# Optimization experiments

Measured on AMD Instinct MI355X. Metric: run time of the kernel, lower is better.

The kernel has to match this reference:

```python
import jax, jax.numpy as jnp
import numpy as np

N_NODES = 50000


def gcn_conv(x, W, b, src, dst, n_nodes):
    """PyG GCNConv: h = x @ W; symmetric-normalized aggregation with self-loops; + bias."""
    h = x @ W  # [N, F_out]
    ones = jnp.ones(src.shape[0], dtype=h.dtype)
    # degree including the self-loop (edge weight 1)
    deg = jax.ops.segment_sum(ones, dst, num_segments=n_nodes) + 1.0
    dinv = jax.lax.rsqrt(deg)  # deg >= 1, always valid
    norm = dinv[src] * dinv[dst]  # [E]
    msgs = h[src] * norm[:, None]  # [E, F_out]
    agg = jax.ops.segment_sum(msgs, dst, num_segments=n_nodes)
    agg = agg + h * (dinv * dinv)[:, None]  # self-loop contribution, norm = dinv_i^2
    return agg + b


def setup_inputs() -> dict:
    key = jax.random.key(0)
    ks = jax.random.split(key, 8)
    n, f_in, f_hid, f_out, n_edges = N_NODES, 128, 128, 40, 800000
    x = jax.random.normal(ks[0], (n, f_in), dtype=jnp.float32)
    edge_index = jax.random.randint(ks[1], (2, n_edges), 0, n, dtype=jnp.int64)
    new_edge_indexs = jax.random.randint(ks[2], (2, 1000), 0, n, dtype=jnp.int64)
    # Glorot init like PyG defaults
    s1 = (6.0 / (f_in + f_hid)) ** 0.5
    s2 = (6.0 / (f_hid + f_out)) ** 0.5
    W1 = jax.random.uniform(ks[3], (f_in, f_hid), jnp.float32, -s1, s1)
    b1 = jnp.zeros((f_hid,), jnp.float32)
    W2 = jax.random.uniform(ks[4], (f_hid, f_out), jnp.float32, -s2, s2)
    b2 = jnp.zeros((f_out,), jnp.float32)
    return {"x": x, "W1": W1, "b1": b1, "W2": W2, "b2": b2,
            "edge_index": edge_index, "new_edge_indexs": new_edge_indexs}


def reference(x, W1, b1, W2, b2, edge_index, new_edge_indexs):
    src, dst = edge_index[0], edge_index[1]
    h = gcn_conv(x, W1, b1, src, dst, N_NODES)
    h = jax.nn.relu(h)
    # dropout(p=0.5) is identity in eval mode (training=False)
    h = gcn_conv(h, W2, b2, src, dst, N_NODES)
    return jax.nn.log_softmax(h, axis=-1)
```

## Files before the change

### kernel.cpp

```cpp
#include <hip/hip_runtime.h>
#include <hip/hip_bf16.h>

#define N_NODES 50000
#define N_EDGES 800000
#define F_IN    128
#define F_HID   128
#define F_OUT   40
#define N_TILES (N_NODES / 16)

#define NBIN      98
#define BIN_SHIFT 9
#define EPB       1024
#define CAP       32
#define GBIN_CAP  9216

#define CVT_BLOCKS ((F_IN * F_HID + 48 * F_HID) / 256)

typedef __attribute__((ext_vector_type(8))) short bf16x8;
typedef __attribute__((ext_vector_type(4))) float f32x4;

__device__ __forceinline__ float2 unpack_bf2(unsigned u) {
    float2 r;
    r.x = __uint_as_float(u << 16);
    r.y = __uint_as_float(u & 0xffff0000u);
    return r;
}
__device__ __forceinline__ unsigned pack_bf2(float x, float y) {
    union { unsigned u; __hip_bfloat16 h[2]; } cv;
    cv.h[0] = __float2bfloat16(x);
    cv.h[1] = __float2bfloat16(y);
    return cv.u;
}
__device__ __forceinline__ short bfraw(float v) {
    __hip_bfloat16 h = __float2bfloat16(v);
    return *(short*)&h;
}
__device__ __forceinline__ float bf16u_to_f32(unsigned short us) {
    return __uint_as_float(((unsigned)us) << 16);
}
__device__ __forceinline__ unsigned f32_to_h16(float v) {
    _Float16 h = (_Float16)v;
    return (unsigned)*(unsigned short*)&h;
}
__device__ __forceinline__ float h16_to_f32(unsigned bits) {
    unsigned short us = (unsigned short)bits;
    _Float16 h = *(_Float16*)&us;
    return (float)h;
}

__device__ __forceinline__ int ld_src(const unsigned int* w, int is64, int e) {
    return is64 ? (int)w[2 * e] : (int)w[e];
}
__device__ __forceinline__ int ld_dst(const unsigned int* w, int is64, int e) {
    return is64 ? (int)w[2 * (N_EDGES + e)] : (int)w[N_EDGES + e];
}

__global__ void k_init(const unsigned int* __restrict__ ew,
                       const float* __restrict__ W1, const float* __restrict__ W2,
                       __hip_bfloat16* __restrict__ w1t, __hip_bfloat16* __restrict__ w2t,
                       int* __restrict__ flag, int* __restrict__ gcnt) {
    int b = blockIdx.x, t = threadIdx.x;
    if (b < CVT_BLOCKS) {
        int idx = b * 256 + t;
        if (idx < F_IN * F_HID) {
            int n = idx >> 7, k = idx & 127;
            w1t[idx] = __float2bfloat16(W1[k * F_HID + n]);
        } else {
            int j = idx - F_IN * F_HID;
            int n = j >> 7, k = j & 127;
            w2t[j] = __float2bfloat16(n < F_OUT ? W2[k * F_OUT + n] : 0.f);
        }
        return;
    }
    __shared__ int nz;
    if (t == 0) nz = 0;
    __syncthreads();
    int local = 0;
    for (int i = t; i < 4096; i += 256)
        if (ew[2 * i + 1] != 0u) local = 1;
    if (local) atomicOr(&nz, 1);
    if (t < NBIN) gcnt[t] = 0;
    __syncthreads();
    if (t == 0) flag[0] = (nz == 0) ? 1 : 0;
}

__global__ void k_bin(const unsigned int* __restrict__ ew, const int* __restrict__ flag,
                      int* __restrict__ gcnt, unsigned* __restrict__ gbin) {
    __shared__ unsigned buf[NBIN][CAP];
    __shared__ int cnt[NBIN];
    __shared__ int base[NBIN];
    int t = threadIdx.x;
    for (int i = t; i < NBIN; i += 256) cnt[i] = 0;
    __syncthreads();
    int is64 = flag[0];
    int e0 = blockIdx.x * EPB;
    int n = min(EPB, N_EDGES - e0);
    for (int i = t; i < n; i += 256) {
        int e = e0 + i;
        int s = ld_src(ew, is64, e), d = ld_dst(ew, is64, e);
        unsigned rec = (unsigned)s | ((unsigned)d << 16);
        int b = d >> BIN_SHIFT;
        int c = atomicAdd(&cnt[b], 1);
        if (c < CAP) buf[b][c] = rec;
        else {
            int g = atomicAdd(&gcnt[b], 1);
            gbin[(size_t)b * GBIN_CAP + g] = rec;
        }
    }
    __syncthreads();
    if (t < NBIN) {
        int m = min(cnt[t], CAP);
        base[t] = atomicAdd(&gcnt[t], m);
        cnt[t] = m;
    }
    __syncthreads();
    int wave = t >> 6, lane = t & 63;
    for (int b = wave; b < NBIN; b += 4) {
        int m = cnt[b], bs = base[b];
        for (int i = lane; i < m; i += 64)
            gbin[(size_t)b * GBIN_CAP + bs + i] = buf[b][i];
    }
}

__global__ void k_passB1(const int* __restrict__ gcnt, const unsigned* __restrict__ gbin,
                         int* __restrict__ rowptr, float* __restrict__ dinv) {
    __shared__ int c[512];
    __shared__ int s2[256];
    __shared__ int gall[NBIN];
    __shared__ int bbase;
    int t = threadIdx.x;
    int b = blockIdx.x;
    c[t] = 0; c[t + 256] = 0;
    if (t < NBIN) gall[t] = gcnt[t];
    __syncthreads();
    if (t == 0) {
        int s = 0;
        for (int i = 0; i < b; i++) s += gall[i];
        bbase = s;
    }
    int n = gall[b];
    const unsigned* rec = gbin + (size_t)b * GBIN_CAP;
    int base512 = b << BIN_SHIFT;
    for (int i = t; i < n; i += 256)
        atomicAdd(&c[(int)(rec[i] >> 16) - base512], 1);
    __syncthreads();
    int a0 = c[2 * t], a1 = c[2 * t + 1];
    s2[t] = a0 + a1;
    __syncthreads();
    for (int off = 1; off < 256; off <<= 1) {
        int u = (t >= off) ? s2[t - off] : 0;
        __syncthreads();
        s2[t] += u;
        __syncthreads();
    }
    int ebase = bbase + s2[t] - a0 - a1;
    int i0 = base512 + 2 * t, i1 = i0 + 1;
    if (i0 < N_NODES) { rowptr[i0] = ebase;      dinv[i0] = rsqrtf((float)a0 + 1.f); }
    if (i1 < N_NODES) { rowptr[i1] = ebase + a0; dinv[i1] = rsqrtf((float)a1 + 1.f); }
    if (b == 0 && t == 0) rowptr[N_NODES] = N_EDGES;
}

__global__ void k_passB2(const int* __restrict__ gcnt, const unsigned* __restrict__ gbin,
                         const int* __restrict__ rowptr, const float* __restrict__ dinv,
                         unsigned* __restrict__ srcw) {
    __shared__ int pos[512];
    __shared__ float dloc[512];
    int t = threadIdx.x;
    int b = blockIdx.x;
    int base512 = b << BIN_SHIFT;
#pragma unroll
    for (int k = 0; k < 2; k++) {
        int j = t + k * 256;
        int i = base512 + j;
        pos[j]  = (i < N_NODES) ? rowptr[i] : 0;
        dloc[j] = (i < N_NODES) ? dinv[i] : 0.f;
    }
    __syncthreads();
    int n = gcnt[b];
    const unsigned* rec = gbin + (size_t)b * GBIN_CAP;
    for (int i = t; i < n; i += 256) {
        unsigned r = rec[i];
        int s  = (int)(r & 0xFFFFu);
        int dl = (int)(r >> 16) - base512;
        int slot = atomicAdd(&pos[dl], 1);
        float norm = dinv[s] * dloc[dl];
        srcw[slot] = (unsigned)s | (f32_to_h16(norm) << 16);
    }
}

__global__ void k_gemm1m(const float* __restrict__ x,
                         const __hip_bfloat16* __restrict__ w1t,
                         __hip_bfloat16* __restrict__ h1b) {
    int wave = threadIdx.x >> 6, lane = threadIdx.x & 63;
    int tile = blockIdx.x * 4 + wave;
    if (tile >= N_TILES) return;
    int node0 = tile * 16;
    int m = lane & 15, q = lane >> 4;
    bf16x8 A[4];
    const float* arow = x + (size_t)(node0 + m) * F_IN + q * 8;
#pragma unroll
    for (int kt = 0; kt < 4; kt++) {
        float4 f0 = *(const float4*)(arow + kt * 32);
        float4 f1 = *(const float4*)(arow + kt * 32 + 4);
        bf16x8 a;
        a[0] = bfraw(f0.x); a[1] = bfraw(f0.y); a[2] = bfraw(f0.z); a[3] = bfraw(f0.w);
        a[4] = bfraw(f1.x); a[5] = bfraw(f1.y); a[6] = bfraw(f1.z); a[7] = bfraw(f1.w);
        A[kt] = a;
    }
#pragma unroll
    for (int c = 0; c < 8; c++) {
        f32x4 acc = {0.f, 0.f, 0.f, 0.f};
        const __hip_bfloat16* brow = w1t + (size_t)(c * 16 + m) * F_IN + q * 8;
#pragma unroll
        for (int kt = 0; kt < 4; kt++) {
            bf16x8 B = *(const bf16x8*)(brow + kt * 32);
            acc = __builtin_amdgcn_mfma_f32_16x16x32_bf16(A[kt], B, acc, 0, 0, 0);
        }
#pragma unroll
        for (int r = 0; r < 4; r++)
            h1b[(size_t)(node0 + q * 4 + r) * F_HID + c * 16 + m] = __float2bfloat16(acc[r]);
    }
}

__global__ void k_agg1f(const int* __restrict__ rowptr, const unsigned* __restrict__ srcw,
                        const float* __restrict__ dinv, const __hip_bfloat16* __restrict__ h1b,
                        const float* __restrict__ b1, __hip_bfloat16* __restrict__ h1rb) {
    int wave = threadIdx.x >> 6, lane = threadIdx.x & 63;
    int node = blockIdx.x * 4 + wave;
    float di = dinv[node];
    int beg = rowptr[node], end = rowptr[node + 1];
    const unsigned* h1u = (const unsigned*)h1b;
    float2 acc = unpack_bf2(h1u[(size_t)node * 64 + lane]);
    float w0 = di * di;
    acc.x *= w0; acc.y *= w0;
    int e = beg;
    for (; e + 3 < end; e += 4) {
        unsigned p0 = srcw[e], p1 = srcw[e + 1], p2 = srcw[e + 2], p3 = srcw[e + 3];
        unsigned u0 = h1u[(size_t)(p0 & 0xFFFF) * 64 + lane];
        unsigned u1 = h1u[(size_t)(p1 & 0xFFFF) * 64 + lane];
        unsigned u2 = h1u[(size_t)(p2 & 0xFFFF) * 64 + lane];
        unsigned u3 = h1u[(size_t)(p3 & 0xFFFF) * 64 + lane];
        float w0e = h16_to_f32(p0 >> 16);
        float w1e = h16_to_f32(p1 >> 16);
        float w2e = h16_to_f32(p2 >> 16);
        float w3e = h16_to_f32(p3 >> 16);
        float2 v0 = unpack_bf2(u0), v1 = unpack_bf2(u1), v2 = unpack_bf2(u2), v3 = unpack_bf2(u3);
        acc.x += v0.x * w0e + v1.x * w1e + v2.x * w2e + v3.x * w3e;
        acc.y += v0.y * w0e + v1.y * w1e + v2.y * w2e + v3.y * w3e;
    }
    for (; e < end; e++) {
        unsigned p = srcw[e];
        float w = h16_to_f32(p >> 16);
        float2 v = unpack_bf2(h1u[(size_t)(p & 0xFFFF) * 64 + lane]);
        acc.x += v.x * w;
        acc.y += v.y * w;
    }
    float2 bb = ((const float2*)b1)[lane];
    acc.x = fmaxf(acc.x + bb.x, 0.f);
    acc.y = fmaxf(acc.y + bb.y, 0.f);
    ((unsigned*)h1rb)[(size_t)node * 64 + lane] = pack_bf2(acc.x, acc.y);
}

__global__ void k_gemm2m(const __hip_bfloat16* __restrict__ h1rb,
                         const __hip_bfloat16* __restrict__ w2t,
                         __hip_bfloat16* __restrict__ h2b) {
    int wave = threadIdx.x >> 6, lane = threadIdx.x & 63;
    int tile = blockIdx.x * 4 + wave;
    if (tile >= N_TILES) return;
    int node0 = tile * 16;
    int m = lane & 15, q = lane >> 4;
    bf16x8 A[4];
    const __hip_bfloat16* arow = h1rb + (size_t)(node0 + m) * F_HID + q * 8;
#pragma unroll
    for (int kt = 0; kt < 4; kt++)
        A[kt] = *(const bf16x8*)(arow + kt * 32);
#pragma unroll
    for (int c = 0; c < 3; c++) {
        f32x4 acc = {0.f, 0.f, 0.f, 0.f};
        const __hip_bfloat16* brow = w2t + (size_t)(c * 16 + m) * F_HID + q * 8;
#pragma unroll
        for (int kt = 0; kt < 4; kt++) {
            bf16x8 B = *(const bf16x8*)(brow + kt * 32);
            acc = __builtin_amdgcn_mfma_f32_16x16x32_bf16(A[kt], B, acc, 0, 0, 0);
        }
        int col = c * 16 + m;
        if (col < F_OUT) {
#pragma unroll
            for (int r = 0; r < 4; r++)
                h2b[(size_t)(node0 + q * 4 + r) * F_OUT + col] = __float2bfloat16(acc[r]);
        }
    }
}

__global__ void k_agg2f(const int* __restrict__ rowptr, const unsigned* __restrict__ srcw,
                        const float* __restrict__ dinv,
                        const unsigned short* __restrict__ h2b,
                        const float* __restrict__ b2, float* __restrict__ out) {
    int wave = threadIdx.x >> 6, lane = threadIdx.x & 63;
    int node = blockIdx.x * 4 + wave;
    float di = dinv[node];
    int beg = rowptr[node], end = rowptr[node + 1];
    int l = (lane < F_OUT) ? lane : 0;
    float acc = bf16u_to_f32(h2b[(size_t)node * F_OUT + l]) * di * di;
    int e = beg;
    for (; e + 3 < end; e += 4) {
        unsigned p0 = srcw[e], p1 = srcw[e + 1], p2 = srcw[e + 2], p3 = srcw[e + 3];
        float v0 = bf16u_to_f32(h2b[(size_t)(p0 & 0xFFFF) * F_OUT + l]);
        float v1 = bf16u_to_f32(h2b[(size_t)(p1 & 0xFFFF) * F_OUT + l]);
        float v2 = bf16u_to_f32(h2b[(size_t)(p2 & 0xFFFF) * F_OUT + l]);
        float v3 = bf16u_to_f32(h2b[(size_t)(p3 & 0xFFFF) * F_OUT + l]);
        acc += v0 * h16_to_f32(p0 >> 16) + v1 * h16_to_f32(p1 >> 16)
             + v2 * h16_to_f32(p2 >> 16) + v3 * h16_to_f32(p3 >> 16);
    }
    for (; e < end; e++) {
        unsigned p = srcw[e];
        acc += bf16u_to_f32(h2b[(size_t)(p & 0xFFFF) * F_OUT + l]) * h16_to_f32(p >> 16);
    }
    float v = (lane < F_OUT) ? acc + b2[lane] : -INFINITY;
    float m = v;
    for (int off = 32; off; off >>= 1) m = fmaxf(m, __shfl_xor(m, off));
    float ex = (lane < F_OUT) ? __expf(v - m) : 0.f;
    float ssum = ex;
    for (int off = 32; off; off >>= 1) ssum += __shfl_xor(ssum, off);
    float ls = __logf(ssum);
    if (lane < F_OUT)
        out[(size_t)node * F_OUT + lane] = v - m - ls;
}

extern "C" void kernel_launch(void* const* d_in, const int* in_sizes, int n_in,
                              void* d_out, int out_size, void* d_ws, size_t ws_size,
                              hipStream_t stream) {
    const float* x  = (const float*)d_in[0];
    const float* W1 = (const float*)d_in[1];
    const float* b1 = (const float*)d_in[2];
    const float* W2 = (const float*)d_in[3];
    const float* b2 = (const float*)d_in[4];
    const unsigned int* ew = (const unsigned int*)d_in[5];
    float* out = (float*)d_out;

    char* ws = (char*)d_ws;
    int*   flag     = (int*)ws;   ws += 256;
    int*   gcnt     = (int*)ws;   ws += 512;
    float* dinv     = (float*)ws; ws += ((N_NODES * 4 + 255) / 256) * 256;
    int*   rowptr   = (int*)ws;   ws += (((N_NODES + 1) * 4 + 255) / 256) * 256;
    unsigned* gbin  = (unsigned*)ws; ws += (size_t)NBIN * GBIN_CAP * 4;
    unsigned* srcw  = (unsigned*)ws; ws += (size_t)N_EDGES * 4;
    __hip_bfloat16* w1t  = (__hip_bfloat16*)ws; ws += F_IN * F_HID * 2;
    __hip_bfloat16* w2t  = (__hip_bfloat16*)ws; ws += 48 * F_HID * 2;
    __hip_bfloat16* h1b  = (__hip_bfloat16*)ws; ws += (size_t)N_NODES * F_HID * 2;
    __hip_bfloat16* h1rb = (__hip_bfloat16*)ws; ws += (size_t)N_NODES * F_HID * 2;
    __hip_bfloat16* h2b  = (__hip_bfloat16*)ws; ws += (size_t)N_NODES * F_OUT * 2;

    k_init   <<<CVT_BLOCKS + 1, 256, 0, stream>>>(ew, W1, W2, w1t, w2t, flag, gcnt);
    k_bin    <<<(N_EDGES + EPB - 1) / EPB, 256, 0, stream>>>(ew, flag, gcnt, gbin);
    k_passB1 <<<NBIN, 256, 0, stream>>>(gcnt, gbin, rowptr, dinv);
    k_passB2 <<<NBIN, 256, 0, stream>>>(gcnt, gbin, rowptr, dinv, srcw);
    k_gemm1m <<<(N_TILES + 3) / 4, 256, 0, stream>>>(x, w1t, h1b);
    k_agg1f  <<<N_NODES / 4, 256, 0, stream>>>(rowptr, srcw, dinv, h1b, b1, h1rb);
    k_gemm2m <<<(N_TILES + 3) / 4, 256, 0, stream>>>(h1rb, w2t, h2b);
    k_agg2f  <<<N_NODES / 4, 256, 0, stream>>>(rowptr, srcw, dinv,
                                               (const unsigned short*)h2b, b2, out);
}
```

Measured before the change: 234.6 us.

## Fuse GEMM1 into binning kernel and feature-slice layer-1 aggregation

Merges the first GEMM into the edge-binning launch as extra blocks, so the two independent stages share one launch and can overlap. h1 is stored as four 32-feature slices, each node-major. Layer-1 aggregation now runs one pass per slice, with each wave splitting edges across four 16-lane subgroups and combining them with shuffle reductions. The slicing is meant to keep each slice's gather working set small enough to stay cache-resident, at the cost of reading the CSR edge list four times and doing extra shuffles.

```diff
diff --git a/kernel.cpp b/kernel.cpp
--- a/kernel.cpp
+++ b/kernel.cpp
@@ -15,6 +15,9 @@
 #define GBIN_CAP  9216
 
 #define CVT_BLOCKS ((F_IN * F_HID + 48 * F_HID) / 256)
+#define BIN_BLOCKS ((N_EDGES + EPB - 1) / EPB)
+#define G1_BLOCKS  ((N_TILES + 3) / 4)
+#define AGG1_NB    (N_NODES / 4)
 
 typedef __attribute__((ext_vector_type(8))) short bf16x8;
 typedef __attribute__((ext_vector_type(4))) float f32x4;
@@ -84,41 +87,78 @@
     if (t == 0) flag[0] = (nz == 0) ? 1 : 0;
 }
 
-__global__ void k_bin(const unsigned int* __restrict__ ew, const int* __restrict__ flag,
-                      int* __restrict__ gcnt, unsigned* __restrict__ gbin) {
+__global__ void k_bing1(const unsigned int* __restrict__ ew, const int* __restrict__ flag,
+                        int* __restrict__ gcnt, unsigned* __restrict__ gbin,
+                        const float* __restrict__ x, const __hip_bfloat16* __restrict__ w1t,
+                        __hip_bfloat16* __restrict__ h1b) {
     __shared__ unsigned buf[NBIN][CAP];
     __shared__ int cnt[NBIN];
     __shared__ int base[NBIN];
     int t = threadIdx.x;
-    for (int i = t; i < NBIN; i += 256) cnt[i] = 0;
-    __syncthreads();
-    int is64 = flag[0];
-    int e0 = blockIdx.x * EPB;
-    int n = min(EPB, N_EDGES - e0);
-    for (int i = t; i < n; i += 256) {
-        int e = e0 + i;
-        int s = ld_src(ew, is64, e), d = ld_dst(ew, is64, e);
-        unsigned rec = (unsigned)s | ((unsigned)d << 16);
-        int b = d >> BIN_SHIFT;
-        int c = atomicAdd(&cnt[b], 1);
-        if (c < CAP) buf[b][c] = rec;
-        else {
-            int g = atomicAdd(&gcnt[b], 1);
-            gbin[(size_t)b * GBIN_CAP + g] = rec;
-        }
-    }
-    __syncthreads();
-    if (t < NBIN) {
-        int m = min(cnt[t], CAP);
-        base[t] = atomicAdd(&gcnt[t], m);
-        cnt[t] = m;
-    }
-    __syncthreads();
+    if (blockIdx.x < BIN_BLOCKS) {
+        for (int i = t; i < NBIN; i += 256) cnt[i] = 0;
+        __syncthreads();
+        int is64 = flag[0];
+        int e0 = blockIdx.x * EPB;
+        int n = min(EPB, N_EDGES - e0);
+        for (int i = t; i < n; i += 256) {
+            int e = e0 + i;
+            int s = ld_src(ew, is64, e), d = ld_dst(ew, is64, e);
+            unsigned rec = (unsigned)s | ((unsigned)d << 16);
+            int b = d >> BIN_SHIFT;
+            int c = atomicAdd(&cnt[b], 1);
+            if (c < CAP) buf[b][c] = rec;
+            else {
+                int g = atomicAdd(&gcnt[b], 1);
+                gbin[(size_t)b * GBIN_CAP + g] = rec;
+            }
+        }
+        __syncthreads();
+        if (t < NBIN) {
+            int m = min(cnt[t], CAP);
+            base[t] = atomicAdd(&gcnt[t], m);
+            cnt[t] = m;
+        }
+        __syncthreads();
+        int wave = t >> 6, lane = t & 63;
+        for (int b = wave; b < NBIN; b += 4) {
+            int m = cnt[b], bs = base[b];
+            for (int i = lane; i < m; i += 64)
+                gbin[(size_t)b * GBIN_CAP + bs + i] = buf[b][i];
+        }
+        return;
+    }
     int wave = t >> 6, lane = t & 63;
-    for (int b = wave; b < NBIN; b += 4) {
-        int m = cnt[b], bs = base[b];
-        for (int i = lane; i < m; i += 64)
-            gbin[(size_t)b * GBIN_CAP + bs + i] = buf[b][i];
+    int tile = (blockIdx.x - BIN_BLOCKS) * 4 + wave;
+    if (tile >= N_TILES) return;
+    int node0 = tile * 16;
+    int m = lane & 15, q = lane >> 4;
+    bf16x8 A[4];
+    const float* arow = x + (size_t)(node0 + m) * F_IN + q * 8;
+#pragma unroll
+    for (int kt = 0; kt < 4; kt++) {
+        float4 f0 = *(const float4*)(arow + kt * 32);
+        float4 f1 = *(const float4*)(arow + kt * 32 + 4);
+        bf16x8 a;
+        a[0] = bfraw(f0.x); a[1] = bfraw(f0.y); a[2] = bfraw(f0.z); a[3] = bfraw(f0.w);
+        a[4] = bfraw(f1.x); a[5] = bfraw(f1.y); a[6] = bfraw(f1.z); a[7] = bfraw(f1.w);
+        A[kt] = a;
+    }
+#pragma unroll
+    for (int c = 0; c < 8; c++) {
+        f32x4 acc = {0.f, 0.f, 0.f, 0.f};
+        const __hip_bfloat16* brow = w1t + (size_t)(c * 16 + m) * F_IN + q * 8;
+#pragma unroll
+        for (int kt = 0; kt < 4; kt++) {
+            bf16x8 B = *(const bf16x8*)(brow + kt * 32);
+            acc = __builtin_amdgcn_mfma_f32_16x16x32_bf16(A[kt], B, acc, 0, 0, 0);
+        }
+        int feat = c * 16 + m;
+        int pass = feat >> 5, fs = feat & 31;
+#pragma unroll
+        for (int r = 0; r < 4; r++)
+            h1b[(size_t)pass * N_NODES * 32 + (size_t)(node0 + q * 4 + r) * 32 + fs] =
+                __float2bfloat16(acc[r]);
     }
 }
 
@@ -188,77 +228,39 @@
     }
 }
 
-__global__ void k_gemm1m(const float* __restrict__ x,
-                         const __hip_bfloat16* __restrict__ w1t,
-                         __hip_bfloat16* __restrict__ h1b) {
-    int wave = threadIdx.x >> 6, lane = threadIdx.x & 63;
-    int tile = blockIdx.x * 4 + wave;
-    if (tile >= N_TILES) return;
-    int node0 = tile * 16;
-    int m = lane & 15, q = lane >> 4;
-    bf16x8 A[4];
-    const float* arow = x + (size_t)(node0 + m) * F_IN + q * 8;
-#pragma unroll
-    for (int kt = 0; kt < 4; kt++) {
-        float4 f0 = *(const float4*)(arow + kt * 32);
-        float4 f1 = *(const float4*)(arow + kt * 32 + 4);
-        bf16x8 a;
-        a[0] = bfraw(f0.x); a[1] = bfraw(f0.y); a[2] = bfraw(f0.z); a[3] = bfraw(f0.w);
-        a[4] = bfraw(f1.x); a[5] = bfraw(f1.y); a[6] = bfraw(f1.z); a[7] = bfraw(f1.w);
-        A[kt] = a;
-    }
-#pragma unroll
-    for (int c = 0; c < 8; c++) {
-        f32x4 acc = {0.f, 0.f, 0.f, 0.f};
-        const __hip_bfloat16* brow = w1t + (size_t)(c * 16 + m) * F_IN + q * 8;
-#pragma unroll
-        for (int kt = 0; kt < 4; kt++) {
-            bf16x8 B = *(const bf16x8*)(brow + kt * 32);
-            acc = __builtin_amdgcn_mfma_f32_16x16x32_bf16(A[kt], B, acc, 0, 0, 0);
-        }
-#pragma unroll
-        for (int r = 0; r < 4; r++)
-            h1b[(size_t)(node0 + q * 4 + r) * F_HID + c * 16 + m] = __float2bfloat16(acc[r]);
-    }
-}
-
-__global__ void k_agg1f(const int* __restrict__ rowptr, const unsigned* __restrict__ srcw,
+__global__ void k_agg1s(const int* __restrict__ rowptr, const unsigned* __restrict__ srcw,
                         const float* __restrict__ dinv, const __hip_bfloat16* __restrict__ h1b,
                         const float* __restrict__ b1, __hip_bfloat16* __restrict__ h1rb) {
     int wave = threadIdx.x >> 6, lane = threadIdx.x & 63;
-    int node = blockIdx.x * 4 + wave;
-    float di = dinv[node];
+    int pass = blockIdx.x / AGG1_NB;
+    int node = (blockIdx.x % AGG1_NB) * 4 + wave;
+    int sub = lane >> 4, f2 = lane & 15;
+    const unsigned* slice = (const unsigned*)h1b + (size_t)pass * N_NODES * 16;
     int beg = rowptr[node], end = rowptr[node + 1];
-    const unsigned* h1u = (const unsigned*)h1b;
-    float2 acc = unpack_bf2(h1u[(size_t)node * 64 + lane]);
-    float w0 = di * di;
-    acc.x *= w0; acc.y *= w0;
-    int e = beg;
-    for (; e + 3 < end; e += 4) {
-        unsigned p0 = srcw[e], p1 = srcw[e + 1], p2 = srcw[e + 2], p3 = srcw[e + 3];
-        unsigned u0 = h1u[(size_t)(p0 & 0xFFFF) * 64 + lane];
-        unsigned u1 = h1u[(size_t)(p1 & 0xFFFF) * 64 + lane];
-        unsigned u2 = h1u[(size_t)(p2 & 0xFFFF) * 64 + lane];
-        unsigned u3 = h1u[(size_t)(p3 & 0xFFFF) * 64 + lane];
-        float w0e = h16_to_f32(p0 >> 16);
-        float w1e = h16_to_f32(p1 >> 16);
-        float w2e = h16_to_f32(p2 >> 16);
-        float w3e = h16_to_f32(p3 >> 16);
-        float2 v0 = unpack_bf2(u0), v1 = unpack_bf2(u1), v2 = unpack_bf2(u2), v3 = unpack_bf2(u3);
-        acc.x += v0.x * w0e + v1.x * w1e + v2.x * w2e + v3.x * w3e;
-        acc.y += v0.y * w0e + v1.y * w1e + v2.y * w2e + v3.y * w3e;
-    }
-    for (; e < end; e++) {
-        unsigned p = srcw[e];
-        float w = h16_to_f32(p >> 16);
-        float2 v = unpack_bf2(h1u[(size_t)(p & 0xFFFF) * 64 + lane]);
-        acc.x += v.x * w;
-        acc.y += v.y * w;
-    }
-    float2 bb = ((const float2*)b1)[lane];
-    acc.x = fmaxf(acc.x + bb.x, 0.f);
-    acc.y = fmaxf(acc.y + bb.y, 0.f);
-    ((unsigned*)h1rb)[(size_t)node * 64 + lane] = pack_bf2(acc.x, acc.y);
+    float accx = 0.f, accy = 0.f;
+    for (int e = beg; e < end; e += 8) {
+        int e0 = e + sub, e1 = e + 4 + sub;
+        bool ok0 = e0 < end, ok1 = e1 < end;
+        unsigned p0 = ok0 ? srcw[e0] : 0u;
+        unsigned p1 = ok1 ? srcw[e1] : 0u;
+        float2 v0 = {0.f, 0.f}, v1 = {0.f, 0.f};
+        if (ok0) v0 = unpack_bf2(slice[(size_t)(p0 & 0xFFFFu) * 16 + f2]);
+        if (ok1) v1 = unpack_bf2(slice[(size_t)(p1 & 0xFFFFu) * 16 + f2]);
+        float w0 = ok0 ? h16_to_f32(p0 >> 16) : 0.f;
+        float w1 = ok1 ? h16_to_f32(p1 >> 16) : 0.f;
+        accx += v0.x * w0 + v1.x * w1;
+        accy += v0.y * w0 + v1.y * w1;
+    }
+    accx += __shfl_xor(accx, 16); accy += __shfl_xor(accy, 16);
+    accx += __shfl_xor(accx, 32); accy += __shfl_xor(accy, 32);
+    if (sub == 0) {
+        float di = dinv[node];
+        float2 self = unpack_bf2(slice[(size_t)node * 16 + f2]);
+        float2 bb = ((const float2*)b1)[pass * 16 + f2];
+        float ax = fmaxf(accx + self.x * di * di + bb.x, 0.f);
+        float ay = fmaxf(accy + self.y * di * di + bb.y, 0.f);
+        ((unsigned*)h1rb)[(size_t)node * 64 + pass * 16 + f2] = pack_bf2(ax, ay);
+    }
 }
 
 __global__ void k_gemm2m(const __hip_bfloat16* __restrict__ h1rb,
@@ -352,11 +354,10 @@
     __hip_bfloat16* h2b  = (__hip_bfloat16*)ws; ws += (size_t)N_NODES * F_OUT * 2;
 
     k_init   <<<CVT_BLOCKS + 1, 256, 0, stream>>>(ew, W1, W2, w1t, w2t, flag, gcnt);
-    k_bin    <<<(N_EDGES + EPB - 1) / EPB, 256, 0, stream>>>(ew, flag, gcnt, gbin);
+    k_bing1  <<<BIN_BLOCKS + G1_BLOCKS, 256, 0, stream>>>(ew, flag, gcnt, gbin, x, w1t, h1b);
     k_passB1 <<<NBIN, 256, 0, stream>>>(gcnt, gbin, rowptr, dinv);
     k_passB2 <<<NBIN, 256, 0, stream>>>(gcnt, gbin, rowptr, dinv, srcw);
-    k_gemm1m <<<(N_TILES + 3) / 4, 256, 0, stream>>>(x, w1t, h1b);
-    k_agg1f  <<<N_NODES / 4, 256, 0, stream>>>(rowptr, srcw, dinv, h1b, b1, h1rb);
+    k_agg1s  <<<4 * AGG1_NB, 256, 0, stream>>>(rowptr, srcw, dinv, h1b, b1, h1rb);
     k_gemm2m <<<(N_TILES + 3) / 4, 256, 0, stream>>>(h1rb, w2t, h2b);
     k_agg2f  <<<N_NODES / 4, 256, 0, stream>>>(rowptr, srcw, dinv,
                                                (const unsigned short*)h2b, b2, out);
```

Result: slower. 276.8 us (+18.0%).
